# Kernel tuning notes

Hardware: AMD Instinct MI355X
Metric: run time of the kernel (lower is better)

## Reference

```python
import jax, jax.numpy as jnp
import numpy as np

FP8_MAX = 448.0  # e4m3fn saturation value

def q8(x):
    """Round-to-nearest-even quantization to float8 e4m3fn values (kept in fp32).
    Normal min exponent -6, mantissa 3 bits, subnormal step 2^-9, saturate at 448."""
    a = jnp.abs(x)
    e = jnp.clip(jnp.floor(jnp.log2(jnp.maximum(a, 1e-30))), -6.0, 8.0)
    step = jnp.exp2(e - 3.0)  # mantissa quantization step for this binade
    q = jnp.minimum(jnp.round(a / step) * step, FP8_MAX)  # jnp.round is half-to-even
    return jnp.sign(x) * q

def setup_inputs() -> dict:
    key = jax.random.key(0)
    k1, k2, k3 = jax.random.split(key, 3)
    B, D_IN, D_H, D_OUT = 8192, 1024, 4096, 1024
    x = jax.random.normal(k1, (B, D_IN), jnp.float32)
    # learned weights (torch Linear layout: [out, in]); scaled to a realistic FP8 range
    w1 = jax.random.normal(k2, (D_H, D_IN), jnp.float32) * 0.03
    w2 = jax.random.normal(k3, (D_OUT, D_H), jnp.float32) * 0.03
    return {"x": x, "w1": w1, "w2": w2}

def reference(x, w1, w2):
    # x -> fp8 e4m3fn -> bit-pulse encode (lossless round trip for fp8 values)
    x8 = q8(x)
    # spike FP8 linear layers carry fp8 weights (set_weight_from_float quantizes)
    w1q = q8(w1)
    w2q = q8(w2)
    # fc1: spike spatial-encoding adder == accumulate wide, emit FP8 pulses
    h = q8(jnp.einsum('bi,hi->bh', x8, w1q))
    # SpikeFP8ReLU: zero out negative fp8 pulse values
    h = jnp.where(h > 0, h, 0.0)
    # fc2 then fp8_bits_to_float decode
    out = q8(jnp.einsum('bh,oh->bo', h, w2q))
    return out
```

## Files before the change

### kernel.cpp

```cpp
#include <hip/hip_runtime.h>
#include <stdint.h>
#include <stddef.h>

typedef int v4i  __attribute__((ext_vector_type(4)));
typedef int v16i __attribute__((ext_vector_type(16)));

#define KCH  256
#define BUFB (128 * 256)
#define LDSB (2 * BUFB)

__device__ __forceinline__ void gl_lds16(const uint8_t* g, uint8_t* l) {
    __builtin_amdgcn_global_load_lds(
        (const __attribute__((address_space(1))) uint32_t*)g,
        (__attribute__((address_space(3))) uint32_t*)l,
        16, 0, 0);
}

__device__ __forceinline__ float q8f(float v) {
    float a = fabsf(v);
    int e = (int)(__float_as_uint(a) >> 23) - 127;
    e = e < -6 ? -6 : (e > 8 ? 8 : e);
    float step  = __uint_as_float((uint32_t)(e - 3 + 127) << 23);
    float rstep = __uint_as_float((uint32_t)(3 - e + 127) << 23);
    float q = fminf(rintf(a * rstep) * step, 448.0f);
    return v < 0.0f ? -q : q;
}
__device__ __forceinline__ int qm(float v) {
    return (int)rintf(q8f(v) * 512.0f);
}

__device__ __forceinline__ uint32_t rne_sh(uint32_t a, int s) {
    uint32_t t = a >> s;
    uint32_t rem = a & ((1u << s) - 1u);
    uint32_t half = 1u << (s - 1);
    t += (rem > half) || (rem == half && (t & 1u));
    return t;
}

__global__ __launch_bounds__(256) void quant_all_kernel(
    const float* __restrict__ x,  uint32_t* __restrict__ xh, uint32_t* __restrict__ xl,
    const float* __restrict__ w1, uint32_t* __restrict__ w1m,
    const float* __restrict__ w2, uint32_t* __restrict__ w2m,
    int n4x, int n4w1, int n4w2) {
    int i = blockIdx.x * 256 + threadIdx.x;
    if (i < n4x) {
        float4 v = ((const float4*)x)[i];
        int m0 = qm(v.x), m1 = qm(v.y), m2 = qm(v.z), m3 = qm(v.w);
        uint32_t h = ((uint32_t)((m0 >> 5) & 0xff)) | ((uint32_t)((m1 >> 5) & 0xff) << 8) |
                     ((uint32_t)((m2 >> 5) & 0xff) << 16) | ((uint32_t)((m3 >> 5) & 0xff) << 24);
        uint32_t l = ((uint32_t)(m0 & 31)) | ((uint32_t)(m1 & 31) << 8) |
                     ((uint32_t)(m2 & 31) << 16) | ((uint32_t)(m3 & 31) << 24);
        int r = i >> 8, c4 = i & 255;
        int pi = ((r >> 5) * 64 + (c4 >> 2)) * 128 + (r & 31) * 4 + (c4 & 3);
        xh[pi] = h;
        xl[pi] = l;
    } else if (i < n4x + n4w1) {
        int j = i - n4x;
        float4 v = ((const float4*)w1)[j];
        w1m[j] = ((uint32_t)(qm(v.x) & 0xff)) | ((uint32_t)(qm(v.y) & 0xff) << 8) |
                 ((uint32_t)(qm(v.z) & 0xff) << 16) | ((uint32_t)(qm(v.w) & 0xff) << 24);
    } else if (i < n4x + n4w1 + n4w2) {
        int j = i - n4x - n4w1;
        float4 v = ((const float4*)w2)[j];
        w2m[j] = ((uint32_t)(qm(v.x) & 0xff)) | ((uint32_t)(qm(v.y) & 0xff) << 8) |
                 ((uint32_t)(qm(v.z) & 0xff) << 16) | ((uint32_t)(qm(v.w) & 0xff) << 24);
    }
}

__device__ __forceinline__ void stage_chunk(
    const uint8_t* __restrict__ Bm, uint8_t* dst,
    int bn, int K, int kc, int wave, int lane) {
    const int r0 = lane >> 4;
    const int sl = lane & 15;
#pragma unroll
    for (int s = 0; s < 8; ++s) {
        const int qd  = wave * 8 + s;
        const int row = qd * 4 + r0;
        const int g   = sl ^ (row & 15);
        gl_lds16(Bm + (size_t)(bn * 128 + row) * K + kc + g * 16,
                 dst + qd * 1024 + lane * 16);
    }
}

template <int EPI>
__global__ __launch_bounds__(256, 2) void gemm_i8_big(
    const uint8_t* __restrict__ Ah, const uint8_t* __restrict__ Al,
    const uint8_t* __restrict__ Bm,
    void* __restrict__ Ch, void* __restrict__ Cl,
    int M, int N, int K) {
    extern __shared__ uint8_t sB[];

    const int tid  = threadIdx.x;
    const int lane = tid & 63;
    const int wave = tid >> 6;
    const int col  = lane & 31;
    const int kh   = lane >> 5;
    const int xm   = col & 15;

    const int bid = blockIdx.x;
    const int bm  = ((bid & 7) << 3) | ((bid >> 3) & 7);
    const int bn  = (((bid >> 9) << 3) | ((bid >> 6) & 7));

    v16i acc[2][4];
#pragma unroll
    for (int p = 0; p < 2; ++p)
#pragma unroll
        for (int j = 0; j < 4; ++j) acc[p][j] = (v16i)0;

    const size_t abase = (size_t)(bm * 4 + wave) * (K >> 4) * 512 + lane * 16;
    const uint8_t* pAh = Ah + abase;
    const uint8_t* pAl = Al + abase;
    const int NT = K >> 5;

    int rowoff[4];
#pragma unroll
    for (int j = 0; j < 4; ++j) rowoff[j] = (j * 32 + col) * 256;

    const int NC = K / KCH;
    stage_chunk(Bm, sB, bn, K, 0, wave, lane);

    v4i a0 = *(const v4i*)(pAh);
    v4i a1 = *(const v4i*)(pAl);

    for (int c = 0; c < NC; ++c) {
        __syncthreads();
        if (c + 1 < NC)
            stage_chunk(Bm, sB + ((c + 1) & 1) * BUFB, bn, K, (c + 1) * KCH, wave, lane);

        const uint8_t* buf = sB + (c & 1) * BUFB;
#pragma unroll
        for (int t = 0; t < 8; ++t) {
            const int gt = c * 8 + t;
            v4i na0 = a0, na1 = a1;
            if (gt + 1 < NT) {
                na0 = *(const v4i*)(pAh + (size_t)(gt + 1) * 1024);
                na1 = *(const v4i*)(pAl + (size_t)(gt + 1) * 1024);
            }
            const int slot = ((2 * t + kh) & 15) ^ xm;
            v4i b[4];
#pragma unroll
            for (int j = 0; j < 4; ++j)
                b[j] = *(const v4i*)(buf + rowoff[j] + slot * 16);
#pragma unroll
            for (int j = 0; j < 4; ++j) {
                acc[0][j] = __builtin_amdgcn_mfma_i32_32x32x32_i8(a0, b[j], acc[0][j], 0, 0, 0);
                acc[1][j] = __builtin_amdgcn_mfma_i32_32x32x32_i8(a1, b[j], acc[1][j], 0, 0, 0);
            }
            a0 = na0; a1 = na1;
        }
    }

    const int Gn = N >> 4;
    const int rb = bm * 4 + wave;
#pragma unroll
    for (int j = 0; j < 4; ++j) {
        const int colk = bn * 128 + j * 32 + col;
#pragma unroll
        for (int reg = 0; reg < 16; ++reg) {
            int mt = acc[0][j][reg] * 32 + acc[1][j][reg];
            const int rw = 4 * kh + (reg & 3) + 8 * (reg >> 2);
            if (EPI == 0) {
                uint8_t hb = 0, lb = 0;
                if (mt > 0) {
                    int s = 28 - __builtin_clz((uint32_t)mt);
                    if (s < 9) s = 9;
                    int mh = (int)(rne_sh((uint32_t)mt, s) << (s - 9));
                    hb = (uint8_t)(mh >> 5);
                    lb = (uint8_t)(mh & 31);
                }
                size_t pa = ((size_t)rb * Gn + (colk >> 4)) * 512 + rw * 16 + (colk & 15);
                ((uint8_t*)Ch)[pa] = hb;
                ((uint8_t*)Cl)[pa] = lb;
            } else {
                uint32_t a = mt < 0 ? (uint32_t)(-mt) : (uint32_t)mt;
                float v = 0.0f;
                if (a) {
                    int s = 28 - __builtin_clz(a);
                    if (s < 9) s = 9;
                    v = (float)(rne_sh(a, s) << s) * 0x1p-18f;
                    if (mt < 0) v = -v;
                }
                ((float*)Ch)[(size_t)(rb * 32 + rw) * N + colk] = v;
            }
        }
    }
}

extern "C" void kernel_launch(void* const* d_in, const int* in_sizes, int n_in,
                              void* d_out, int out_size, void* d_ws, size_t ws_size,
                              hipStream_t stream) {
    const int Bsz = 8192, DIN = 1024, DH = 4096, DOUT = 1024;
    const float* x  = (const float*)d_in[0];
    const float* w1 = (const float*)d_in[1];
    const float* w2 = (const float*)d_in[2];
    float* out = (float*)d_out;

    uint8_t* ws  = (uint8_t*)d_ws;
    uint8_t* xh  = ws;
    uint8_t* xl  = xh  + (size_t)Bsz * DIN;
    uint8_t* w1m = xl  + (size_t)Bsz * DIN;
    uint8_t* w2m = w1m + (size_t)DH  * DIN;
    uint8_t* hh  = w2m + (size_t)DOUT * DH;
    uint8_t* hl  = hh  + (size_t)Bsz * DH;

    static bool attr_done = false;
    if (!attr_done) {
        hipFuncSetAttribute((const void*)gemm_i8_big<0>,
                            hipFuncAttributeMaxDynamicSharedMemorySize, LDSB);
        hipFuncSetAttribute((const void*)gemm_i8_big<1>,
                            hipFuncAttributeMaxDynamicSharedMemorySize, LDSB);
        attr_done = true;
    }

    const int n4x = Bsz * DIN / 4, n4w1 = DH * DIN / 4, n4w2 = DOUT * DH / 4;
    quant_all_kernel<<<(n4x + n4w1 + n4w2) / 256, 256, 0, stream>>>(
        x, (uint32_t*)xh, (uint32_t*)xl, w1, (uint32_t*)w1m, w2, (uint32_t*)w2m,
        n4x, n4w1, n4w2);

    gemm_i8_big<0><<<dim3(2048), 256, LDSB, stream>>>(xh, xl, w1m, (void*)hh, (void*)hl, Bsz, DH, DIN);

    gemm_i8_big<1><<<dim3(512), 256, LDSB, stream>>>(hh, hl, w2m, (void*)out, nullptr, Bsz, DOUT, DH);
}
```

Baseline: 261.0 us.

## Triple-buffer B tiles with smaller K chunks and batch A fragment loads

Shrinks the LDS K-chunk from 256 to 128 bytes and uses three rotating buffers, prefetching two chunks ahead instead of one. Replaces __syncthreads with a raw s_barrier plus a manual vmcnt wait, and updates the swizzle to the narrower rows. Register double-buffering of A fragments is replaced by loading all four A tiles for a chunk at its start. The aim is to hide more global-load latency and cut LDS from 64KB to 48KB. In exchange it relies on in-order vmcnt behaviour for correctness, uses more registers for A, and synchronises more often.

```diff
diff --git a/kernel.cpp b/kernel.cpp
--- a/kernel.cpp
+++ b/kernel.cpp
@@ -5,9 +5,12 @@
 typedef int v4i  __attribute__((ext_vector_type(4)));
 typedef int v16i __attribute__((ext_vector_type(16)));
 
-#define KCH  256
-#define BUFB (128 * 256)
-#define LDSB (2 * BUFB)
+#define KCH  128
+#define BUFB (128 * 128)
+#define NBUF 3
+#define LDSB (NBUF * BUFB)
+
+#define FENCE() asm volatile("" ::: "memory")
 
 __device__ __forceinline__ void gl_lds16(const uint8_t* g, uint8_t* l) {
     __builtin_amdgcn_global_load_lds(
@@ -70,13 +73,13 @@
 __device__ __forceinline__ void stage_chunk(
     const uint8_t* __restrict__ Bm, uint8_t* dst,
     int bn, int K, int kc, int wave, int lane) {
-    const int r0 = lane >> 4;
-    const int sl = lane & 15;
-#pragma unroll
-    for (int s = 0; s < 8; ++s) {
-        const int qd  = wave * 8 + s;
-        const int row = qd * 4 + r0;
-        const int g   = sl ^ (row & 15);
+    const int r0 = lane >> 3;
+    const int sl = lane & 7;
+#pragma unroll
+    for (int s = 0; s < 4; ++s) {
+        const int qd  = wave * 4 + s;
+        const int row = qd * 8 + r0;
+        const int g   = sl ^ r0;
         gl_lds16(Bm + (size_t)(bn * 128 + row) * K + kc + g * 16,
                  dst + qd * 1024 + lane * 16);
     }
@@ -95,7 +98,7 @@
     const int wave = tid >> 6;
     const int col  = lane & 31;
     const int kh   = lane >> 5;
-    const int xm   = col & 15;
+    const int x7   = col & 7;
 
     const int bid = blockIdx.x;
     const int bm  = ((bid & 7) << 3) | ((bid >> 3) & 7);
@@ -110,43 +113,50 @@
     const size_t abase = (size_t)(bm * 4 + wave) * (K >> 4) * 512 + lane * 16;
     const uint8_t* pAh = Ah + abase;
     const uint8_t* pAl = Al + abase;
-    const int NT = K >> 5;
 
     int rowoff[4];
 #pragma unroll
-    for (int j = 0; j < 4; ++j) rowoff[j] = (j * 32 + col) * 256;
+    for (int j = 0; j < 4; ++j) rowoff[j] = (j * 32 + col) * 128;
 
     const int NC = K / KCH;
+
     stage_chunk(Bm, sB, bn, K, 0, wave, lane);
-
-    v4i a0 = *(const v4i*)(pAh);
-    v4i a1 = *(const v4i*)(pAl);
+    stage_chunk(Bm, sB + BUFB, bn, K, KCH, wave, lane);
+    FENCE();
+    asm volatile("s_waitcnt vmcnt(4)" ::: "memory");
 
     for (int c = 0; c < NC; ++c) {
-        __syncthreads();
-        if (c + 1 < NC)
-            stage_chunk(Bm, sB + ((c + 1) & 1) * BUFB, bn, K, (c + 1) * KCH, wave, lane);
-
-        const uint8_t* buf = sB + (c & 1) * BUFB;
-#pragma unroll
-        for (int t = 0; t < 8; ++t) {
-            const int gt = c * 8 + t;
-            v4i na0 = a0, na1 = a1;
-            if (gt + 1 < NT) {
-                na0 = *(const v4i*)(pAh + (size_t)(gt + 1) * 1024);
-                na1 = *(const v4i*)(pAl + (size_t)(gt + 1) * 1024);
-            }
-            const int slot = ((2 * t + kh) & 15) ^ xm;
+        FENCE();
+        __builtin_amdgcn_s_barrier();
+        FENCE();
+
+        const uint8_t* buf  = sB + (c % NBUF) * BUFB;
+        const uint8_t* pAhc = pAh + (size_t)c * 4096;
+        const uint8_t* pAlc = pAl + (size_t)c * 4096;
+
+        v4i ab[8];
+#pragma unroll
+        for (int u = 0; u < 4; ++u) {
+            ab[2 * u]     = *(const v4i*)(pAhc + u * 1024);
+            ab[2 * u + 1] = *(const v4i*)(pAlc + u * 1024);
+        }
+        FENCE();
+        if (c + 2 < NC)
+            stage_chunk(Bm, sB + ((c + 2) % NBUF) * BUFB, bn, K, (c + 2) * KCH, wave, lane);
+        FENCE();
+
+#pragma unroll
+        for (int t = 0; t < 4; ++t) {
+            const int slot = ((2 * t + kh) ^ x7);
             v4i b[4];
 #pragma unroll
             for (int j = 0; j < 4; ++j)
                 b[j] = *(const v4i*)(buf + rowoff[j] + slot * 16);
 #pragma unroll
             for (int j = 0; j < 4; ++j) {
-                acc[0][j] = __builtin_amdgcn_mfma_i32_32x32x32_i8(a0, b[j], acc[0][j], 0, 0, 0);
-                acc[1][j] = __builtin_amdgcn_mfma_i32_32x32x32_i8(a1, b[j], acc[1][j], 0, 0, 0);
+                acc[0][j] = __builtin_amdgcn_mfma_i32_32x32x32_i8(ab[2 * t],     b[j], acc[0][j], 0, 0, 0);
+                acc[1][j] = __builtin_amdgcn_mfma_i32_32x32x32_i8(ab[2 * t + 1], b[j], acc[1][j], 0, 0, 0);
             }
-            a0 = na0; a1 = na1;
         }
     }
 
```

Measured after the change: 253.2 us. 3.0% less time.
